# Kernel optimization log

Hardware: AMD Instinct MI355X
Metric: run time of the kernel (lower is better)

## Reference

```python
import jax, jax.numpy as jnp
import numpy as np

E = 1024
F = 4096
B = 4
S = 2048

def _layernorm(x, g, b, eps=1e-5):
    mu = jnp.mean(x, axis=-1, keepdims=True)
    var = jnp.var(x, axis=-1, keepdims=True)
    return (x - mu) * jax.lax.rsqrt(var + eps) * g + b

def _attention(q, k, v, Wq, bq, Wk, bk, Wv, bv, Wo, bo, mask=None):
    # single-head attention, scores scaled by sqrt(embed_dim)
    Q = q @ Wq.T + bq
    K = k @ Wk.T + bk
    V = v @ Wv.T + bv
    scores = jnp.einsum('bqe,bke->bqk', Q, K) / jnp.sqrt(jnp.asarray(E, Q.dtype))
    if mask is not None:
        scores = jnp.where(mask, scores, -jnp.inf)
    attn = jax.nn.softmax(scores, axis=-1)
    out = jnp.einsum('bqk,bke->bqe', attn, V)
    return out @ Wo.T + bo

def setup_inputs() -> dict:
    key = jax.random.key(0)
    ks = jax.random.split(key, 20)
    s = 0.02
    d = {
        'src_encs': jax.random.normal(ks[0], (B, S, E), jnp.float32),
        'tgt_embs': jax.random.normal(ks[1], (B, S, E), jnp.float32),
        'ln1_g': jnp.ones((E,), jnp.float32), 'ln1_b': jnp.zeros((E,), jnp.float32),
        'ln2_g': jnp.ones((E,), jnp.float32), 'ln2_b': jnp.zeros((E,), jnp.float32),
        'ln3_g': jnp.ones((E,), jnp.float32), 'ln3_b': jnp.zeros((E,), jnp.float32),
        'sa_Wq': jax.random.normal(ks[2], (E, E), jnp.float32) * s, 'sa_bq': jnp.zeros((E,), jnp.float32),
        'sa_Wk': jax.random.normal(ks[3], (E, E), jnp.float32) * s, 'sa_bk': jnp.zeros((E,), jnp.float32),
        'sa_Wv': jax.random.normal(ks[4], (E, E), jnp.float32) * s, 'sa_bv': jnp.zeros((E,), jnp.float32),
        'sa_Wo': jax.random.normal(ks[5], (E, E), jnp.float32) * s, 'sa_bo': jnp.zeros((E,), jnp.float32),
        'ca_Wq': jax.random.normal(ks[6], (E, E), jnp.float32) * s, 'ca_bq': jnp.zeros((E,), jnp.float32),
        'ca_Wk': jax.random.normal(ks[7], (E, E), jnp.float32) * s, 'ca_bk': jnp.zeros((E,), jnp.float32),
        'ca_Wv': jax.random.normal(ks[8], (E, E), jnp.float32) * s, 'ca_bv': jnp.zeros((E,), jnp.float32),
        'ca_Wo': jax.random.normal(ks[9], (E, E), jnp.float32) * s, 'ca_bo': jnp.zeros((E,), jnp.float32),
        'ff_W1': jax.random.normal(ks[10], (F, E), jnp.float32) * s, 'ff_b1': jnp.zeros((F,), jnp.float32),
        'ff_W2': jax.random.normal(ks[11], (E, F), jnp.float32) * s, 'ff_b2': jnp.zeros((E,), jnp.float32),
    }
    return d

def reference(src_encs, tgt_embs,
              ln1_g, ln1_b, ln2_g, ln2_b, ln3_g, ln3_b,
              sa_Wq, sa_bq, sa_Wk, sa_bk, sa_Wv, sa_bv, sa_Wo, sa_bo,
              ca_Wq, ca_bq, ca_Wk, ca_bk, ca_Wv, ca_bv, ca_Wo, ca_bo,
              ff_W1, ff_b1, ff_W2, ff_b2):
    seq_len = tgt_embs.shape[1]
    causal_mask = jnp.tril(jnp.ones((1, seq_len, seq_len), dtype=bool))
    x_norm = _layernorm(tgt_embs, ln1_g, ln1_b)
    sa = _attention(x_norm, x_norm, x_norm, sa_Wq, sa_bq, sa_Wk, sa_bk, sa_Wv, sa_bv, sa_Wo, sa_bo, mask=causal_mask)
    attn = tgt_embs + sa
    attn_norm = _layernorm(attn, ln2_g, ln2_b)
    ca = _attention(attn_norm, src_encs, src_encs, ca_Wq, ca_bq, ca_Wk, ca_bk, ca_Wv, ca_bv, ca_Wo, ca_bo)
    cross = attn + ca
    cross_norm = _layernorm(cross, ln3_g, ln3_b)
    h = jax.nn.relu(cross_norm @ ff_W1.T + ff_b1)
    ff = h @ ff_W2.T + ff_b2
    return cross + ff
```

## Files before the change

### kernel.cpp

```cpp
#include <hip/hip_runtime.h>
#include <hip/hip_bf16.h>
#include <cstdint>
#include <cstddef>

#define EDIM 1024
#define FDIM 4096
#define BDIM 4
#define SDIM 2048
#define MTOK (BDIM * SDIM)
#define PLD 4096

typedef __bf16 bf16_t;
typedef __bf16 bf16x8 __attribute__((ext_vector_type(8)));
typedef float f32x4 __attribute__((ext_vector_type(4)));

__device__ __forceinline__ void gload_lds16(const void* g, void* l) {
  __builtin_amdgcn_global_load_lds(
      (const __attribute__((address_space(1))) void*)g,
      (__attribute__((address_space(3))) void*)l, 16, 0, 0);
}

__device__ __forceinline__ unsigned short bfbits(float f) {
  bf16_t h = (bf16_t)f;
  return __builtin_bit_cast(unsigned short, h);
}

template <typename OutT, bool BIAS, bool RES, bool RELU, bool CSKIP, bool CKLIM>
__global__ __launch_bounds__(256, 2) void gemm_nt(
    const bf16_t* __restrict__ A, const bf16_t* __restrict__ Bm,
    const float* __restrict__ bias, const float* res,
    OutT* C, int N, int K, int lda, int ldb, int ldc,
    long long sA, long long sB, long long sC, float alpha) {
  const int bn = blockIdx.x, bm = blockIdx.y, bz = blockIdx.z;
  const int m0 = bm * 128, n0 = bn * 128;
  if constexpr (CSKIP) {
    if (n0 > m0 + 127) return;
  }
  A += (size_t)bz * sA;
  Bm += (size_t)bz * sB;
  C += (size_t)bz * sC;

  __shared__ __align__(16) bf16_t As[128][64];
  __shared__ __align__(16) bf16_t Bs[128][64];

  const int tid = threadIdx.x;
  const int lane = tid & 63;
  const int wid = tid >> 6;
  const int wr = (wid >> 1) * 64;
  const int wc = (wid & 1) * 64;
  const int lr = lane & 15;
  const int lk = (lane >> 4) * 8;

  f32x4 acc[4][4] = {};

  int Keff = K;
  if constexpr (CKLIM) {
    const int kl = m0 + 128;
    Keff = kl < K ? kl : K;
  }
  const int nkt = Keff >> 6;

  const int se = tid * 8;
  const int sr = se >> 6;
  const int sc = se & 63;

  for (int kt = 0; kt < nkt; ++kt) {
    const int k0 = kt << 6;
    const bf16_t* Ag = A + (size_t)(m0 + sr) * lda + k0 + sc;
    const bf16_t* Bg = Bm + (size_t)(n0 + sr) * ldb + k0 + sc;
#pragma unroll
    for (int it = 0; it < 4; ++it) {
      gload_lds16(Ag + (size_t)it * 32 * lda, &As[sr + it * 32][sc]);
      gload_lds16(Bg + (size_t)it * 32 * ldb, &Bs[sr + it * 32][sc]);
    }
    __syncthreads();
#pragma unroll
    for (int kk = 0; kk < 2; ++kk) {
      bf16x8 af[4], bfr[4];
#pragma unroll
      for (int i = 0; i < 4; ++i)
        af[i] = *(const bf16x8*)&As[wr + i * 16 + lr][kk * 32 + lk];
#pragma unroll
      for (int i = 0; i < 4; ++i)
        bfr[i] = *(const bf16x8*)&Bs[wc + i * 16 + lr][kk * 32 + lk];
#pragma unroll
      for (int mi = 0; mi < 4; ++mi)
#pragma unroll
        for (int ni = 0; ni < 4; ++ni)
          acc[mi][ni] = __builtin_amdgcn_mfma_f32_16x16x32_bf16(
              af[mi], bfr[ni], acc[mi][ni], 0, 0, 0);
    }
    __syncthreads();
  }

  const int rbase = (lane >> 4) * 4;
#pragma unroll
  for (int mi = 0; mi < 4; ++mi) {
#pragma unroll
    for (int ni = 0; ni < 4; ++ni) {
      const int gc = n0 + wc + ni * 16 + lr;
      float bv = 0.0f;
      if constexpr (BIAS) bv = bias[gc];
#pragma unroll
      for (int j = 0; j < 4; ++j) {
        const int gr = m0 + wr + mi * 16 + rbase + j;
        float v = acc[mi][ni][j] * alpha + bv;
        if constexpr (RES) v += res[(size_t)gr * ldc + gc];
        if constexpr (RELU) v = fmaxf(v, 0.0f);
        C[(size_t)gr * ldc + gc] = (OutT)v;
      }
    }
  }
}

__global__ __launch_bounds__(256) void ln_kernel(const float* __restrict__ x,
                                                 const float* __restrict__ g,
                                                 const float* __restrict__ be,
                                                 bf16_t* __restrict__ y) {
  const int row = blockIdx.x;
  const int t = threadIdx.x;
  const float4 v = ((const float4*)(x + (size_t)row * EDIM))[t];
  float s = v.x + v.y + v.z + v.w;
  float s2 = v.x * v.x + v.y * v.y + v.z * v.z + v.w * v.w;
#pragma unroll
  for (int o = 32; o > 0; o >>= 1) {
    s += __shfl_xor(s, o, 64);
    s2 += __shfl_xor(s2, o, 64);
  }
  __shared__ float red[8];
  const int wid = t >> 6;
  if ((t & 63) == 0) {
    red[wid] = s;
    red[4 + wid] = s2;
  }
  __syncthreads();
  s = red[0] + red[1] + red[2] + red[3];
  s2 = red[4] + red[5] + red[6] + red[7];
  const float mu = s * (1.0f / EDIM);
  const float var = s2 * (1.0f / EDIM) - mu * mu;
  const float rs = rsqrtf(var + 1e-5f);
  const float4 gg = ((const float4*)g)[t];
  const float4 bb = ((const float4*)be)[t];
  ushort4 o4;
  o4.x = bfbits((v.x - mu) * rs * gg.x + bb.x);
  o4.y = bfbits((v.y - mu) * rs * gg.y + bb.y);
  o4.z = bfbits((v.z - mu) * rs * gg.z + bb.z);
  o4.w = bfbits((v.w - mu) * rs * gg.w + bb.w);
  ((ushort4*)(y + (size_t)row * EDIM))[t] = o4;
}

template <bool CAUSAL>
__global__ __launch_bounds__(256) void softmax_kernel(
    const float* sc, bf16_t* p) {
  const int row = blockIdx.x;
  const int len = CAUSAL ? (row & (SDIM - 1)) + 1 : SDIM;
  const int t = threadIdx.x;
  const float4* srow = (const float4*)(sc + (size_t)row * SDIM);
  const float4 a = srow[t];
  const float4 b = srow[t + 256];
  const int c0 = t * 4, c1 = 1024 + t * 4;
  float xa[4] = {a.x, a.y, a.z, a.w};
  float xb[4] = {b.x, b.y, b.z, b.w};
#pragma unroll
  for (int i = 0; i < 4; ++i) {
    if (c0 + i >= len) xa[i] = -1e30f;
    if (c1 + i >= len) xb[i] = -1e30f;
  }
  float mx = fmaxf(fmaxf(fmaxf(xa[0], xa[1]), fmaxf(xa[2], xa[3])),
                   fmaxf(fmaxf(xb[0], xb[1]), fmaxf(xb[2], xb[3])));
#pragma unroll
  for (int o = 32; o > 0; o >>= 1) mx = fmaxf(mx, __shfl_xor(mx, o, 64));
  __shared__ float red[4];
  const int wid = t >> 6;
  if ((t & 63) == 0) red[wid] = mx;
  __syncthreads();
  mx = fmaxf(fmaxf(red[0], red[1]), fmaxf(red[2], red[3]));
  __syncthreads();
  float sm = 0.0f;
#pragma unroll
  for (int i = 0; i < 4; ++i) {
    xa[i] = __expf(xa[i] - mx);
    xb[i] = __expf(xb[i] - mx);
    sm += xa[i] + xb[i];
  }
#pragma unroll
  for (int o = 32; o > 0; o >>= 1) sm += __shfl_xor(sm, o, 64);
  if ((t & 63) == 0) red[wid] = sm;
  __syncthreads();
  sm = red[0] + red[1] + red[2] + red[3];
  const float inv = 1.0f / sm;
  ushort4 o0, o1;
  o0.x = bfbits(xa[0] * inv);
  o0.y = bfbits(xa[1] * inv);
  o0.z = bfbits(xa[2] * inv);
  o0.w = bfbits(xa[3] * inv);
  o1.x = bfbits(xb[0] * inv);
  o1.y = bfbits(xb[1] * inv);
  o1.z = bfbits(xb[2] * inv);
  o1.w = bfbits(xb[3] * inv);
  ushort4* prow = (ushort4*)(p + (size_t)row * PLD);
  prow[t] = o0;
  prow[t + 256] = o1;
}

__global__ __launch_bounds__(256) void transpose_bf16(
    const bf16_t* __restrict__ in, bf16_t* __restrict__ out, int R, int C,
    int ldin, long long sIn, long long sOut) {
  __shared__ bf16_t tile[32][33];
  const bf16_t* ip = in + (size_t)blockIdx.z * sIn;
  bf16_t* op = out + (size_t)blockIdx.z * sOut;
  const int r0 = blockIdx.y * 32, c0 = blockIdx.x * 32;
  const int tx = threadIdx.x & 31, ty = threadIdx.x >> 5;
#pragma unroll
  for (int i = 0; i < 32; i += 8)
    tile[ty + i][tx] = ip[(size_t)(r0 + ty + i) * ldin + c0 + tx];
  __syncthreads();
#pragma unroll
  for (int i = 0; i < 32; i += 8)
    op[(size_t)(c0 + ty + i) * R + r0 + tx] = tile[tx][ty + i];
}

__global__ __launch_bounds__(256) void cvt_f32_bf16(const float* __restrict__ in,
                                                    bf16_t* __restrict__ out,
                                                    int n4) {
  int i = blockIdx.x * 256 + threadIdx.x;
  const int stride = gridDim.x * 256;
  for (; i < n4; i += stride) {
    const float4 v = ((const float4*)in)[i];
    ushort4 o;
    o.x = bfbits(v.x);
    o.y = bfbits(v.y);
    o.z = bfbits(v.z);
    o.w = bfbits(v.w);
    ((ushort4*)out)[i] = o;
  }
}

__global__ void pack_bias(const float* a, const float* b, const float* c,
                          float* dst, int n) {
  int i = blockIdx.x * 256 + threadIdx.x;
  int total = c ? 3 * n : 2 * n;
  if (i >= total) return;
  const float* src = (i < n) ? a : (i < 2 * n ? b : c);
  dst[i] = src[i % n];
}

extern "C" void kernel_launch(void* const* d_in, const int* in_sizes, int n_in,
                              void* d_out, int out_size, void* d_ws,
                              size_t ws_size, hipStream_t stream) {
  (void)in_sizes;
  (void)n_in;
  (void)out_size;
  (void)ws_size;
  const float* src_encs = (const float*)d_in[0];
  const float* tgt = (const float*)d_in[1];
  const float* ln1_g = (const float*)d_in[2];
  const float* ln1_b = (const float*)d_in[3];
  const float* ln2_g = (const float*)d_in[4];
  const float* ln2_b = (const float*)d_in[5];
  const float* ln3_g = (const float*)d_in[6];
  const float* ln3_b = (const float*)d_in[7];
  const float* sa_Wq = (const float*)d_in[8];
  const float* sa_bq = (const float*)d_in[9];
  const float* sa_Wk = (const float*)d_in[10];
  const float* sa_bk = (const float*)d_in[11];
  const float* sa_Wv = (const float*)d_in[12];
  const float* sa_bv = (const float*)d_in[13];
  const float* sa_Wo = (const float*)d_in[14];
  const float* sa_bo = (const float*)d_in[15];
  const float* ca_Wq = (const float*)d_in[16];
  const float* ca_bq = (const float*)d_in[17];
  const float* ca_Wk = (const float*)d_in[18];
  const float* ca_bk = (const float*)d_in[19];
  const float* ca_Wv = (const float*)d_in[20];
  const float* ca_bv = (const float*)d_in[21];
  const float* ca_Wo = (const float*)d_in[22];
  const float* ca_bo = (const float*)d_in[23];
  const float* ff_W1 = (const float*)d_in[24];
  const float* ff_b1 = (const float*)d_in[25];
  const float* ff_W2 = (const float*)d_in[26];
  const float* ff_b2 = (const float*)d_in[27];
  float* out = (float*)d_out;

  float* resid = out;

  char* w = (char*)d_ws;
  auto take = [&](size_t bytes) {
    void* pp = (void*)w;
    w += (bytes + 255) & ~(size_t)255;
    return pp;
  };
  const size_t TE_BF = (size_t)MTOK * EDIM * 2;
  const size_t EE2 = (size_t)EDIM * EDIM * 2;

  bf16_t* xn = (bf16_t*)take(TE_BF);
  bf16_t* qkv = (bf16_t*)take((size_t)MTOK * 3 * EDIM * 2);
  bf16_t* vt = (bf16_t*)take(TE_BF);
  bf16_t* srcb = (bf16_t*)take(TE_BF);
  float* sc = (float*)take((size_t)BDIM * SDIM * SDIM * 4);
  bf16_t* wqkv = (bf16_t*)take(3 * EE2);
  bf16_t* cwq = (bf16_t*)take(EE2);
  bf16_t* cwkv = (bf16_t*)take(2 * EE2);
  bf16_t* wo = (bf16_t*)take(EE2);
  bf16_t* cwo = (bf16_t*)take(EE2);
  bf16_t* w1 = (bf16_t*)take((size_t)FDIM * EDIM * 2);
  bf16_t* w2 = (bf16_t*)take((size_t)EDIM * FDIM * 2);
  float* bqkv = (float*)take(3 * EDIM * 4);
  float* cbkv = (float*)take(2 * EDIM * 4);
  bf16_t* pbx = (bf16_t*)sc;
  bf16_t* aox = (bf16_t*)sc + 2048;
  bf16_t* h = (bf16_t*)sc;

  const int EE4 = EDIM * EDIM / 4;
  const int FE4 = FDIM * EDIM / 4;
  cvt_f32_bf16<<<1024, 256, 0, stream>>>(sa_Wq, wqkv, EE4);
  cvt_f32_bf16<<<1024, 256, 0, stream>>>(sa_Wk, wqkv + EDIM * EDIM, EE4);
  cvt_f32_bf16<<<1024, 256, 0, stream>>>(sa_Wv, wqkv + 2 * EDIM * EDIM, EE4);
  cvt_f32_bf16<<<1024, 256, 0, stream>>>(ca_Wq, cwq, EE4);
  cvt_f32_bf16<<<1024, 256, 0, stream>>>(ca_Wk, cwkv, EE4);
  cvt_f32_bf16<<<1024, 256, 0, stream>>>(ca_Wv, cwkv + EDIM * EDIM, EE4);
  cvt_f32_bf16<<<1024, 256, 0, stream>>>(sa_Wo, wo, EE4);
  cvt_f32_bf16<<<1024, 256, 0, stream>>>(ca_Wo, cwo, EE4);
  cvt_f32_bf16<<<2048, 256, 0, stream>>>(ff_W1, w1, FE4);
  cvt_f32_bf16<<<2048, 256, 0, stream>>>(ff_W2, w2, FE4);
  cvt_f32_bf16<<<2048, 256, 0, stream>>>(src_encs, srcb, MTOK * EDIM / 4);
  pack_bias<<<12, 256, 0, stream>>>(sa_bq, sa_bk, sa_bv, bqkv, EDIM);
  pack_bias<<<8, 256, 0, stream>>>(ca_bk, ca_bv, nullptr, cbkv, EDIM);

  const int LQKV = 3 * EDIM;
  const long long sQ = (long long)SDIM * LQKV;
  const long long sS = (long long)SDIM * SDIM;
  const long long sP = (long long)SDIM * PLD;
  const long long sVT = (long long)EDIM * SDIM;
  const float asc = 0.03125f;

  ln_kernel<<<MTOK, 256, 0, stream>>>(tgt, ln1_g, ln1_b, xn);
  gemm_nt<bf16_t, true, false, false, false, false>
      <<<dim3(24, 64, 1), 256, 0, stream>>>(xn, wqkv, bqkv, nullptr, qkv,
                                            LQKV, EDIM, EDIM, EDIM, LQKV,
                                            0, 0, 0, 1.0f);
  transpose_bf16<<<dim3(32, 64, BDIM), 256, 0, stream>>>(
      qkv + 2 * EDIM, vt, SDIM, EDIM, LQKV, sQ, sVT);
  gemm_nt<float, false, false, false, true, false>
      <<<dim3(16, 16, BDIM), 256, 0, stream>>>(qkv, qkv + EDIM, nullptr,
                                               nullptr, sc, SDIM, EDIM, LQKV,
                                               LQKV, SDIM, sQ, sQ, sS, asc);
  softmax_kernel<true><<<MTOK, 256, 0, stream>>>(sc, pbx);
  gemm_nt<bf16_t, false, false, false, false, true>
      <<<dim3(8, 16, BDIM), 256, 0, stream>>>(pbx, vt, nullptr, nullptr, aox,
                                              EDIM, SDIM, PLD, SDIM, PLD,
                                              sP, sVT, sP, 1.0f);
  gemm_nt<float, true, true, false, false, false>
      <<<dim3(8, 64, 1), 256, 0, stream>>>(aox, wo, sa_bo, tgt, resid, EDIM,
                                           EDIM, PLD, EDIM, EDIM, 0, 0, 0,
                                           1.0f);

  ln_kernel<<<MTOK, 256, 0, stream>>>(resid, ln2_g, ln2_b, xn);
  gemm_nt<bf16_t, true, false, false, false, false>
      <<<dim3(8, 64, 1), 256, 0, stream>>>(xn, cwq, ca_bq, nullptr, qkv,
                                           EDIM, EDIM, EDIM, EDIM, LQKV,
                                           0, 0, 0, 1.0f);
  gemm_nt<bf16_t, true, false, false, false, false>
      <<<dim3(16, 64, 1), 256, 0, stream>>>(srcb, cwkv, cbkv, nullptr,
                                            qkv + EDIM, 2 * EDIM, EDIM, EDIM,
                                            EDIM, LQKV, 0, 0, 0, 1.0f);
  transpose_bf16<<<dim3(32, 64, BDIM), 256, 0, stream>>>(
      qkv + 2 * EDIM, vt, SDIM, EDIM, LQKV, sQ, sVT);
  gemm_nt<float, false, false, false, false, false>
      <<<dim3(16, 16, BDIM), 256, 0, stream>>>(qkv, qkv + EDIM, nullptr,
                                               nullptr, sc, SDIM, EDIM, LQKV,
                                               LQKV, SDIM, sQ, sQ, sS, asc);
  softmax_kernel<false><<<MTOK, 256, 0, stream>>>(sc, pbx);
  gemm_nt<bf16_t, false, false, false, false, false>
      <<<dim3(8, 16, BDIM), 256, 0, stream>>>(pbx, vt, nullptr, nullptr, aox,
                                              EDIM, SDIM, PLD, SDIM, PLD,
                                              sP, sVT, sP, 1.0f);
  gemm_nt<float, true, true, false, false, false>
      <<<dim3(8, 64, 1), 256, 0, stream>>>(aox, cwo, ca_bo, resid, resid,
                                           EDIM, EDIM, PLD, EDIM, EDIM, 0, 0,
                                           0, 1.0f);

  ln_kernel<<<MTOK, 256, 0, stream>>>(resid, ln3_g, ln3_b, xn);
  gemm_nt<bf16_t, true, false, true, false, false>
      <<<dim3(32, 64, 1), 256, 0, stream>>>(xn, w1, ff_b1, nullptr, h, FDIM,
                                            EDIM, EDIM, EDIM, FDIM, 0, 0, 0,
                                            1.0f);
  gemm_nt<float, true, true, false, false, false>
      <<<dim3(8, 64, 1), 256, 0, stream>>>(h, w2, ff_b2, resid, out, EDIM,
                                           FDIM, FDIM, FDIM, EDIM, 0, 0, 0,
                                           1.0f);
}
```

Baseline: 924.4 us.

## Double-buffer GEMM LDS tiles, remap workgroups per XCD, batch weight conversions

Adds an optional double-buffered LDS path to the GEMM, so the global-to-LDS load of the next K tile is issued before the MFMA work on the current tile. It is enabled for a subset of GEMM launches. All GEMMs also get an XCD-aware block index remap that gives each of the eight XCDs a contiguous range of tiles, aiming for better L2 reuse. The eight separate 1024x1024 weight conversion launches are merged into one kernel. Double buffering doubles LDS use per block, which can cut occupancy under launch_bounds(256,2), and the remap adds index arithmetic to every block.

```diff
diff --git a/kernel.cpp b/kernel.cpp
--- a/kernel.cpp
+++ b/kernel.cpp
@@ -25,13 +25,28 @@
   return __builtin_bit_cast(unsigned short, h);
 }
 
-template <typename OutT, bool BIAS, bool RES, bool RELU, bool CSKIP, bool CKLIM>
+__device__ __forceinline__ void xcd_remap(int& bx, int& by, int& bz) {
+  const int gx = gridDim.x, gy = gridDim.y;
+  const int nwg = gx * gy * gridDim.z;
+  int id = blockIdx.x + gx * (blockIdx.y + gy * blockIdx.z);
+  const int q = nwg >> 3, r = nwg & 7;
+  const int xcd = id & 7, off = id >> 3;
+  id = (xcd < r ? xcd * (q + 1) : r * (q + 1) + (xcd - r) * q) + off;
+  bx = id % gx;
+  const int t = id / gx;
+  by = t % gy;
+  bz = t / gy;
+}
+
+template <typename OutT, bool BIAS, bool RES, bool RELU, bool CSKIP,
+          bool CKLIM, bool DBUF>
 __global__ __launch_bounds__(256, 2) void gemm_nt(
     const bf16_t* __restrict__ A, const bf16_t* __restrict__ Bm,
     const float* __restrict__ bias, const float* res,
     OutT* C, int N, int K, int lda, int ldb, int ldc,
     long long sA, long long sB, long long sC, float alpha) {
-  const int bn = blockIdx.x, bm = blockIdx.y, bz = blockIdx.z;
+  int bn, bm, bz;
+  xcd_remap(bn, bm, bz);
   const int m0 = bm * 128, n0 = bn * 128;
   if constexpr (CSKIP) {
     if (n0 > m0 + 127) return;
@@ -40,8 +55,8 @@
   Bm += (size_t)bz * sB;
   C += (size_t)bz * sC;
 
-  __shared__ __align__(16) bf16_t As[128][64];
-  __shared__ __align__(16) bf16_t Bs[128][64];
+  __shared__ __align__(16) bf16_t As[DBUF ? 2 : 1][128][64];
+  __shared__ __align__(16) bf16_t Bs[DBUF ? 2 : 1][128][64];
 
   const int tid = threadIdx.x;
   const int lane = tid & 63;
@@ -64,25 +79,26 @@
   const int sr = se >> 6;
   const int sc = se & 63;
 
-  for (int kt = 0; kt < nkt; ++kt) {
+  auto stage = [&](int buf, int kt) {
     const int k0 = kt << 6;
     const bf16_t* Ag = A + (size_t)(m0 + sr) * lda + k0 + sc;
     const bf16_t* Bg = Bm + (size_t)(n0 + sr) * ldb + k0 + sc;
 #pragma unroll
     for (int it = 0; it < 4; ++it) {
-      gload_lds16(Ag + (size_t)it * 32 * lda, &As[sr + it * 32][sc]);
-      gload_lds16(Bg + (size_t)it * 32 * ldb, &Bs[sr + it * 32][sc]);
+      gload_lds16(Ag + (size_t)it * 32 * lda, &As[buf][sr + it * 32][sc]);
+      gload_lds16(Bg + (size_t)it * 32 * ldb, &Bs[buf][sr + it * 32][sc]);
     }
-    __syncthreads();
+  };
+  auto compute = [&](int buf) {
 #pragma unroll
     for (int kk = 0; kk < 2; ++kk) {
       bf16x8 af[4], bfr[4];
 #pragma unroll
       for (int i = 0; i < 4; ++i)
-        af[i] = *(const bf16x8*)&As[wr + i * 16 + lr][kk * 32 + lk];
+        af[i] = *(const bf16x8*)&As[buf][wr + i * 16 + lr][kk * 32 + lk];
 #pragma unroll
       for (int i = 0; i < 4; ++i)
-        bfr[i] = *(const bf16x8*)&Bs[wc + i * 16 + lr][kk * 32 + lk];
+        bfr[i] = *(const bf16x8*)&Bs[buf][wc + i * 16 + lr][kk * 32 + lk];
 #pragma unroll
       for (int mi = 0; mi < 4; ++mi)
 #pragma unroll
@@ -90,7 +106,26 @@
           acc[mi][ni] = __builtin_amdgcn_mfma_f32_16x16x32_bf16(
               af[mi], bfr[ni], acc[mi][ni], 0, 0, 0);
     }
+  };
+
+  if constexpr (DBUF) {
+    stage(0, 0);
     __syncthreads();
+    int cur = 0;
+    for (int kt = 0; kt < nkt - 1; ++kt) {
+      stage(cur ^ 1, kt + 1);
+      compute(cur);
+      __syncthreads();
+      cur ^= 1;
+    }
+    compute(cur);
+  } else {
+    for (int kt = 0; kt < nkt; ++kt) {
+      stage(0, kt);
+      __syncthreads();
+      compute(0);
+      __syncthreads();
+    }
   }
 
   const int rbase = (lane >> 4) * 4;
@@ -223,6 +258,28 @@
 __global__ __launch_bounds__(256) void cvt_f32_bf16(const float* __restrict__ in,
                                                     bf16_t* __restrict__ out,
                                                     int n4) {
+  int i = blockIdx.x * 256 + threadIdx.x;
+  const int stride = gridDim.x * 256;
+  for (; i < n4; i += stride) {
+    const float4 v = ((const float4*)in)[i];
+    ushort4 o;
+    o.x = bfbits(v.x);
+    o.y = bfbits(v.y);
+    o.z = bfbits(v.z);
+    o.w = bfbits(v.w);
+    ((ushort4*)out)[i] = o;
+  }
+}
+
+struct Ptr8 {
+  const float* p[8];
+};
+__global__ __launch_bounds__(256) void cvt8_f32_bf16(Ptr8 srcs,
+                                                     bf16_t* __restrict__ dst) {
+  const int m = blockIdx.y;
+  const float* in = srcs.p[m];
+  bf16_t* out = dst + (size_t)m * EDIM * EDIM;
+  const int n4 = EDIM * EDIM / 4;
   int i = blockIdx.x * 256 + threadIdx.x;
   const int stride = gridDim.x * 256;
   for (; i < n4; i += stride) {
@@ -298,11 +355,12 @@
   bf16_t* vt = (bf16_t*)take(TE_BF);
   bf16_t* srcb = (bf16_t*)take(TE_BF);
   float* sc = (float*)take((size_t)BDIM * SDIM * SDIM * 4);
-  bf16_t* wqkv = (bf16_t*)take(3 * EE2);
-  bf16_t* cwq = (bf16_t*)take(EE2);
-  bf16_t* cwkv = (bf16_t*)take(2 * EE2);
-  bf16_t* wo = (bf16_t*)take(EE2);
-  bf16_t* cwo = (bf16_t*)take(EE2);
+  bf16_t* w8 = (bf16_t*)take(8 * EE2);
+  bf16_t* wqkv = w8;
+  bf16_t* cwq = w8 + 3 * EDIM * EDIM;
+  bf16_t* cwkv = w8 + 4 * EDIM * EDIM;
+  bf16_t* wo = w8 + 6 * EDIM * EDIM;
+  bf16_t* cwo = w8 + 7 * EDIM * EDIM;
   bf16_t* w1 = (bf16_t*)take((size_t)FDIM * EDIM * 2);
   bf16_t* w2 = (bf16_t*)take((size_t)EDIM * FDIM * 2);
   float* bqkv = (float*)take(3 * EDIM * 4);
@@ -311,16 +369,17 @@
   bf16_t* aox = (bf16_t*)sc + 2048;
   bf16_t* h = (bf16_t*)sc;
 
-  const int EE4 = EDIM * EDIM / 4;
   const int FE4 = FDIM * EDIM / 4;
-  cvt_f32_bf16<<<1024, 256, 0, stream>>>(sa_Wq, wqkv, EE4);
-  cvt_f32_bf16<<<1024, 256, 0, stream>>>(sa_Wk, wqkv + EDIM * EDIM, EE4);
-  cvt_f32_bf16<<<1024, 256, 0, stream>>>(sa_Wv, wqkv + 2 * EDIM * EDIM, EE4);
-  cvt_f32_bf16<<<1024, 256, 0, stream>>>(ca_Wq, cwq, EE4);
-  cvt_f32_bf16<<<1024, 256, 0, stream>>>(ca_Wk, cwkv, EE4);
-  cvt_f32_bf16<<<1024, 256, 0, stream>>>(ca_Wv, cwkv + EDIM * EDIM, EE4);
-  cvt_f32_bf16<<<1024, 256, 0, stream>>>(sa_Wo, wo, EE4);
-  cvt_f32_bf16<<<1024, 256, 0, stream>>>(ca_Wo, cwo, EE4);
+  Ptr8 w8src;
+  w8src.p[0] = sa_Wq;
+  w8src.p[1] = sa_Wk;
+  w8src.p[2] = sa_Wv;
+  w8src.p[3] = ca_Wq;
+  w8src.p[4] = ca_Wk;
+  w8src.p[5] = ca_Wv;
+  w8src.p[6] = sa_Wo;
+  w8src.p[7] = ca_Wo;
+  cvt8_f32_bf16<<<dim3(256, 8), 256, 0, stream>>>(w8src, w8);
   cvt_f32_bf16<<<2048, 256, 0, stream>>>(ff_W1, w1, FE4);
   cvt_f32_bf16<<<2048, 256, 0, stream>>>(ff_W2, w2, FE4);
   cvt_f32_bf16<<<2048, 256, 0, stream>>>(src_encs, srcb, MTOK * EDIM / 4);
@@ -335,57 +394,57 @@
   const float asc = 0.03125f;
 
   ln_kernel<<<MTOK, 256, 0, stream>>>(tgt, ln1_g, ln1_b, xn);
-  gemm_nt<bf16_t, true, false, false, false, false>
+  gemm_nt<bf16_t, true, false, false, false, false, false>
       <<<dim3(24, 64, 1), 256, 0, stream>>>(xn, wqkv, bqkv, nullptr, qkv,
                                             LQKV, EDIM, EDIM, EDIM, LQKV,
                                             0, 0, 0, 1.0f);
   transpose_bf16<<<dim3(32, 64, BDIM), 256, 0, stream>>>(
       qkv + 2 * EDIM, vt, SDIM, EDIM, LQKV, sQ, sVT);
-  gemm_nt<float, false, false, false, true, false>
+  gemm_nt<float, false, false, false, true, false, true>
       <<<dim3(16, 16, BDIM), 256, 0, stream>>>(qkv, qkv + EDIM, nullptr,
                                                nullptr, sc, SDIM, EDIM, LQKV,
                                                LQKV, SDIM, sQ, sQ, sS, asc);
   softmax_kernel<true><<<MTOK, 256, 0, stream>>>(sc, pbx);
-  gemm_nt<bf16_t, false, false, false, false, true>
+  gemm_nt<bf16_t, false, false, false, false, true, true>
       <<<dim3(8, 16, BDIM), 256, 0, stream>>>(pbx, vt, nullptr, nullptr, aox,
                                               EDIM, SDIM, PLD, SDIM, PLD,
                                               sP, sVT, sP, 1.0f);
-  gemm_nt<float, true, true, false, false, false>
+  gemm_nt<float, true, true, false, false, false, true>
       <<<dim3(8, 64, 1), 256, 0, stream>>>(aox, wo, sa_bo, tgt, resid, EDIM,
                                            EDIM, PLD, EDIM, EDIM, 0, 0, 0,
                                            1.0f);
 
   ln_kernel<<<MTOK, 256, 0, stream>>>(resid, ln2_g, ln2_b, xn);
-  gemm_nt<bf16_t, true, false, false, false, false>
+  gemm_nt<bf16_t, true, false, false, false, false, true>
       <<<dim3(8, 64, 1), 256, 0, stream>>>(xn, cwq, ca_bq, nullptr, qkv,
                                            EDIM, EDIM, EDIM, EDIM, LQKV,
                                            0, 0, 0, 1.0f);
-  gemm_nt<bf16_t, true, false, false, false, false>
+  gemm_nt<bf16_t, true, false, false, false, false, false>
       <<<dim3(16, 64, 1), 256, 0, stream>>>(srcb, cwkv, cbkv, nullptr,
                                             qkv + EDIM, 2 * EDIM, EDIM, EDIM,
                                             EDIM, LQKV, 0, 0, 0, 1.0f);
   transpose_bf16<<<dim3(32, 64, BDIM), 256, 0, stream>>>(
       qkv + 2 * EDIM, vt, SDIM, EDIM, LQKV, sQ, sVT);
-  gemm_nt<float, false, false, false, false, false>
+  gemm_nt<float, false, false, false, false, false, false>
       <<<dim3(16, 16, BDIM), 256, 0, stream>>>(qkv, qkv + EDIM, nullptr,
                                                nullptr, sc, SDIM, EDIM, LQKV,
                                                LQKV, SDIM, sQ, sQ, sS, asc);
   softmax_kernel<false><<<MTOK, 256, 0, stream>>>(sc, pbx);
-  gemm_nt<bf16_t, false, false, false, false, false>
+  gemm_nt<bf16_t, false, false, false, false, false, true>
       <<<dim3(8, 16, BDIM), 256, 0, stream>>>(pbx, vt, nullptr, nullptr, aox,
                                               EDIM, SDIM, PLD, SDIM, PLD,
                                               sP, sVT, sP, 1.0f);
-  gemm_nt<float, true, true, false, false, false>
+  gemm_nt<float, true, true, false, false, false, true>
       <<<dim3(8, 64, 1), 256, 0, stream>>>(aox, cwo, ca_bo, resid, resid,
                                            EDIM, EDIM, PLD, EDIM, EDIM, 0, 0,
                                            0, 1.0f);
 
   ln_kernel<<<MTOK, 256, 0, stream>>>(resid, ln3_g, ln3_b, xn);
-  gemm_nt<bf16_t, true, false, true, false, false>
+  gemm_nt<bf16_t, true, false, true, false, false, false>
       <<<dim3(32, 64, 1), 256, 0, stream>>>(xn, w1, ff_b1, nullptr, h, FDIM,
                                             EDIM, EDIM, EDIM, FDIM, 0, 0, 0,
                                             1.0f);
-  gemm_nt<float, true, true, false, false, false>
+  gemm_nt<float, true, true, false, false, false, true>
       <<<dim3(8, 64, 1), 256, 0, stream>>>(h, w2, ff_b2, resid, out, EDIM,
                                            FDIM, FDIM, FDIM, EDIM, 0, 0, 0,
                                            1.0f);
```

Result: slower. 970.4 us (+5.0%).
